# Kernel tuning notes

Hardware: AMD Instinct MI355X
Metric: run time of the kernel (lower is better)

## Reference

```python
import jax, jax.numpy as jnp
import numpy as np

KERNEL_SIZE = 11
SIGMA = 1.5
K1 = 0.01
K2 = 0.03
DATA_RANGE = 1.0


def _gaussian_kernel_2d(kernel_size=KERNEL_SIZE, sigma=SIGMA):
    x = jnp.arange(kernel_size, dtype=jnp.float32) - kernel_size // 2
    k1d = jnp.exp(-0.5 * (x / sigma) ** 2)
    k1d = k1d / k1d.sum()
    k2d = k1d[None, :] * k1d[:, None]
    # OIHW layout, single in/out channel
    return k2d[None, None, :, :]


def _gauss_filter(x, kernel):
    pad = KERNEL_SIZE // 2
    return jax.lax.conv_general_dilated(
        x, kernel,
        window_strides=(1, 1),
        padding=[(pad, pad), (pad, pad)],
        dimension_numbers=('NCHW', 'OIHW', 'NCHW'))


def setup_inputs() -> dict:
    key = jax.random.key(0)
    k1, k2 = jax.random.split(key)
    B, C, H, W = 128, 1, 320, 320
    pred = jax.random.uniform(k1, (B, C, H, W), dtype=jnp.float32)
    target = jax.random.uniform(k2, (B, C, H, W), dtype=jnp.float32)
    return {"pred": pred, "target": target}


def reference(pred, target):
    kernel = _gaussian_kernel_2d()
    mu_x = _gauss_filter(pred, kernel)
    mu_y = _gauss_filter(target, kernel)
    mu_x_sq = mu_x * mu_x
    mu_y_sq = mu_y * mu_y
    mu_xy = mu_x * mu_y
    sigma_x_sq = _gauss_filter(pred * pred, kernel) - mu_x_sq
    sigma_y_sq = _gauss_filter(target * target, kernel) - mu_y_sq
    sigma_xy = _gauss_filter(pred * target, kernel) - mu_xy
    dr = jnp.asarray(DATA_RANGE, dtype=pred.dtype)
    c1 = (K1 * dr) ** 2
    c2 = (K2 * dr) ** 2
    numerator = (2 * mu_xy + c1) * (2 * sigma_xy + c2)
    denominator = (mu_x_sq + mu_y_sq + c1) * (sigma_x_sq + sigma_y_sq + c2)
    ssim_map = numerator / denominator
    return 1.0 - ssim_map.mean()
```

## Files before the change

kernel.cpp:

```cpp
#include <hip/hip_runtime.h>


namespace {
constexpr int W = 320, H = 320, B = 128;
constexpr int TH = 8;
constexpr int NSTRIPE = H / TH;
constexpr int NWAVE = B * NSTRIPE;
constexpr int ITERS = TH / 2;
constexpr float C1 = 1.0e-4f;
constexpr float C2 = 9.0e-4f;
constexpr int NSLOT = 128;
constexpr int SSTR = 16;
}

typedef _Float16 h2 __attribute__((ext_vector_type(2)));
typedef float f4a __attribute__((ext_vector_type(4), aligned(4)));

__device__ __forceinline__ float fdot2f(h2 a, h2 b, float c) {
#if __has_builtin(__builtin_amdgcn_fdot2)
  return __builtin_amdgcn_fdot2(a, b, c, false);
#else
  return fmaf((float)a.x, (float)b.x, fmaf((float)a.y, (float)b.y, c));
#endif
}

__device__ __forceinline__ float rcpf(float x) {
  float r;
  asm("v_rcp_f32 %0, %1" : "=v"(r) : "v"(x));
  return r;
}

__device__ __forceinline__ h2 pack2(float a, float b) {
  return h2{(_Float16)a, (_Float16)b};
}

__device__ __forceinline__ h2 pkrtz(float a, float b) {
#if __has_builtin(__builtin_amdgcn_cvt_pkrtz)
  return __builtin_bit_cast(h2, __builtin_amdgcn_cvt_pkrtz(a, b));
#else
  return pack2(a, b);
#endif
}

__device__ __forceinline__ h2 dpp_up1(h2 v) {
  int r = __builtin_amdgcn_update_dpp(0, __builtin_bit_cast(int, v),
                                      0x138, 0xF, 0xF, true);
  return __builtin_bit_cast(h2, r);
}
__device__ __forceinline__ h2 dpp_dn1(h2 v) {
  int r = __builtin_amdgcn_update_dpp(0, __builtin_bit_cast(int, v),
                                      0x130, 0xF, 0xF, true);
  return __builtin_bit_cast(h2, r);
}

#define LOADROW_V(PTR, A)                                                     \
  do {                                                                        \
    const f4a q_ = *(const f4a*)(PTR);                                        \
    A[0] = q_.x; A[1] = q_.y; A[2] = q_.z; A[3] = q_.w;                       \
    A[4] = (PTR)[4];                                                          \
  } while (0)

#define LOADP_RAW(ROW, A0, B0, A1, B1)                                        \
  do {                                                                        \
    const int r0_ = (ROW);                                                    \
    if (r0_ >= 0 && r0_ < H) {                                                \
      LOADROW_V(P + r0_ * W, A0);                                             \
      LOADROW_V(T + r0_ * W, B0);                                             \
    } else {                                                                  \
      _Pragma("unroll") for (int c_ = 0; c_ < 5; ++c_) {                      \
        A0[c_] = 0.f; B0[c_] = 0.f;                                           \
      }                                                                       \
    }                                                                         \
    if (r0_ + 1 >= 0 && r0_ + 1 < H) {                                        \
      LOADROW_V(P + (r0_ + 1) * W, A1);                                       \
      LOADROW_V(T + (r0_ + 1) * W, B1);                                       \
    } else {                                                                  \
      _Pragma("unroll") for (int c_ = 0; c_ < 5; ++c_) {                      \
        A1[c_] = 0.f; B1[c_] = 0.f;                                           \
      }                                                                       \
    }                                                                         \
  } while (0)

#define PACKTO(J, A0, B0, A1, B1)                                             \
  do {                                                                        \
    _Pragma("unroll") for (int c_ = 0; c_ < 5; ++c_) {                        \
      const h2 hp_ = pkrtz(A0[c_], A1[c_]);                                   \
      const h2 ht_ = pkrtz(B0[c_], B1[c_]);                                   \
      rs[J][c_] = (hp_ + ht_) * H05;                                          \
      rd[J][c_] = (hp_ - ht_) * H05;                                          \
    }                                                                         \
  } while (0)

#define HALO(PKc, L, R)                                                       \
  do {                                                                        \
    _Pragma("unroll") for (int c_ = 0; c_ < 5; ++c_) {                        \
      L[c_] = dpp_up1(PKc[c_]);                                               \
      R[c_] = dpp_dn1(PKc[c_]);                                               \
    }                                                                         \
  } while (0)

#define XCOL(PKc, L, R, G)                                                    \
  (((G) < 0) ? L[(G) + 5] : (((G) <= 4) ? PKc[(G)] : R[(G) - 5]))

#define HBLUR9(PKc, L, R, O)                                                  \
  do {                                                                        \
    _Pragma("unroll") for (int c_ = 0; c_ < 5; ++c_) {                        \
      h2 s1_ = W9H[0] * XCOL(PKc, L, R, c_ - 4);                              \
      _Pragma("unroll") for (int k_ = 1; k_ <= 4; ++k_)                       \
        s1_ = W9H[k_] * XCOL(PKc, L, R, c_ - 4 + k_) + s1_;                   \
      h2 s2_ = W9H[8] * XCOL(PKc, L, R, c_ + 4);                              \
      _Pragma("unroll") for (int k_ = 7; k_ >= 5; --k_)                       \
        s2_ = W9H[k_] * XCOL(PKc, L, R, c_ - 4 + k_) + s2_;                   \
      O[c_] = s1_ + s2_;                                                      \
    }                                                                         \
  } while (0)

__global__ __launch_bounds__(64) void ssim_main(
    const float* __restrict__ pred, const float* __restrict__ targ,
    float* __restrict__ sink, int slotmask, int sstr) {
  const int lane = threadIdx.x & 63;
  const int stripe = blockIdx.x;
  const int img = stripe / NSTRIPE;
  const int y0  = (stripe % NSTRIPE) * TH;

  const float* __restrict__ P = pred + (size_t)img * (W * H) + 5 * lane;
  const float* __restrict__ T = targ + (size_t)img * (W * H) + 5 * lane;

  constexpr float W9[9] = {0.00761451f, 0.03607501f, 0.10958607f, 0.21344455f,
                           0.26655996f, 0.21344455f, 0.10958607f, 0.03607501f,
                           0.00761451f};
  const h2 wAv[5] = {pack2(W9[0], W9[1]), pack2(W9[2], W9[3]),
                     pack2(W9[4], W9[5]), pack2(W9[6], W9[7]),
                     pack2(W9[8], 0.f)};
  const h2 wBv[5] = {pack2(0.f, W9[0]),   pack2(W9[1], W9[2]),
                     pack2(W9[3], W9[4]), pack2(W9[5], W9[6]),
                     pack2(W9[7], W9[8])};
  h2 W9H[9];
#pragma unroll
  for (int k = 0; k < 9; ++k) W9H[k] = pack2(W9[k], W9[k]);
  const h2 H05 = pack2(0.5f, 0.5f);

  h2 rs[5][5], rd[5][5];
  float nfA[5], ntA[5], nfB[5], ntB[5];

  {
    float aA[5], bA[5], cA[5], dA[5];
    float aB[5], bB[5], cB[5], dB[5];
    LOADP_RAW(y0 - 4, aA, bA, cA, dA);
    LOADP_RAW(y0 - 2, aB, bB, cB, dB);
    PACKTO(1, aA, bA, cA, dA);
    LOADP_RAW(y0 + 0, aA, bA, cA, dA);
    PACKTO(2, aB, bB, cB, dB);
    LOADP_RAW(y0 + 2, aB, bB, cB, dB);
    PACKTO(3, aA, bA, cA, dA);
    LOADP_RAW(y0 + 4, nfA, ntA, nfB, ntB);
    PACKTO(4, aB, bB, cB, dB);
  }

  float acc = 0.f;

#pragma unroll 1
  for (int it = 0; it < ITERS; ++it) {
#pragma unroll
    for (int j = 0; j < 4; ++j)
#pragma unroll
      for (int c = 0; c < 5; ++c) {
        rs[j][c] = rs[j + 1][c];
        rd[j][c] = rd[j + 1][c];
      }
    PACKTO(4, nfA, ntA, nfB, ntB);
    if (it + 1 < ITERS) LOADP_RAW(y0 + 2 * it + 6, nfA, ntA, nfB, ntB);

    h2 PK[4][5];
#pragma unroll
    for (int c = 0; c < 5; ++c) {
      float sA = 0, dA = 0, ssA = 0, ddA = 0;
      float sB = 0, dB = 0, ssB = 0, ddB = 0;
#pragma unroll
      for (int j = 0; j < 5; ++j) {
        const h2 a = rs[j][c], b = rd[j][c];
        const h2 aa = a * a, bb = b * b;
        const h2 wa = wAv[j], wb = wBv[j];
        sA  = fdot2f(wa, a, sA);
        dA  = fdot2f(wa, b, dA);
        ssA = fdot2f(wa, aa, ssA);
        ddA = fdot2f(wa, bb, ddA);
        sB  = fdot2f(wb, a, sB);
        dB  = fdot2f(wb, b, dB);
        ssB = fdot2f(wb, aa, ssB);
        ddB = fdot2f(wb, bb, ddB);
      }
      PK[0][c] = pkrtz(sA, sB);
      PK[1][c] = pkrtz(dA, dB);
      PK[2][c] = pkrtz(ssA, ssB);
      PK[3][c] = pkrtz(ddA, ddB);
    }

    h2 OUT[4][5];
#pragma unroll
    for (int ch = 0; ch < 4; ++ch) {
      h2 L[5], R[5];
      HALO(PK[ch], L, R);
      HBLUR9(PK[ch], L, R, OUT[ch]);
    }

#pragma unroll
    for (int c = 0; c < 5; ++c) {
#pragma unroll
      for (int r = 0; r < 2; ++r) {
        const float u = r ? (float)OUT[0][c].y : (float)OUT[0][c].x;
        const float v = r ? (float)OUT[1][c].y : (float)OUT[1][c].x;
        const float w = r ? (float)OUT[2][c].y : (float)OUT[2][c].x;
        const float x = r ? (float)OUT[3][c].y : (float)OUT[3][c].x;
        const float uu = u * u, vv = v * v;
        const float A  = uu + vv;
        const float Bq = uu - vv;
        const float num1 = fmaf(2.f, Bq, C1);
        const float num2 = fmaf(2.f, (w - x) - Bq, C2);
        const float den1 = fmaf(2.f, A, C1);
        const float den2 = fmaf(2.f, (w + x) - A, C2);
        acc = fmaf(num1 * num2, rcpf(den1 * den2), acc);
      }
    }
  }

#pragma unroll
  for (int off = 32; off; off >>= 1) acc += __shfl_xor(acc, off, 64);
  if (lane == 0) atomicAdd(sink + (stripe & slotmask) * sstr, acc);
}

__global__ void ssim_final(const float* __restrict__ sink, int nslot, int sstr,
                           float* __restrict__ out) {
  const int tid = threadIdx.x;
  float v = 0.f;
  for (int s = tid; s < nslot; s += 64) v += sink[s * sstr];
#pragma unroll
  for (int off = 32; off; off >>= 1) v += __shfl_xor(v, off, 64);
  if (tid == 0) out[0] = 1.f - v / 13107200.f;
}

extern "C" void kernel_launch(void* const* d_in, const int* in_sizes, int n_in,
                              void* d_out, int out_size, void* d_ws, size_t ws_size,
                              hipStream_t stream) {
  (void)in_sizes; (void)n_in; (void)out_size;
  const float* pred = (const float*)d_in[0];
  const float* targ = (const float*)d_in[1];
  float* out = (float*)d_out;

  float* sink;
  int nslot, sstr;
  const size_t need = (size_t)NSLOT * SSTR * sizeof(float);
  if (ws_size >= need) {
    sink = (float*)d_ws;
    nslot = NSLOT;
    sstr = SSTR;
  } else {
    sink = out;
    nslot = 1;
    sstr = 0;
  }
  (void)hipMemsetAsync(sink, 0, nslot == 1 ? sizeof(float) : need, stream);
  ssim_main<<<dim3(NWAVE), dim3(64), 0, stream>>>(pred, targ, sink, nslot - 1, sstr);
  ssim_final<<<1, 64, 0, stream>>>(sink, nslot, sstr, out);
}
```

Before: 52.17 us.

## Move SSIM final math to packed fp16 and unroll row loop by two

The pointwise SSIM combination now runs on packed half2 operations instead of per-lane fp32. The 0.5 scaling moves from the pack step into the final formula, which removes multiplies from the pack stage. The row loop is restructured to compute two row-pairs per iteration with a 6-deep register window, so the register shift and prefetch happen half as often. The cost is fp16 range and precision risk in the squared and product terms, including possible overflow or accuracy loss for the sum-scaled values, plus higher register pressure.

```diff
diff --git a/kernel.cpp b/kernel.cpp
--- a/kernel.cpp
+++ b/kernel.cpp
@@ -6,7 +6,6 @@
 constexpr int TH = 8;
 constexpr int NSTRIPE = H / TH;
 constexpr int NWAVE = B * NSTRIPE;
-constexpr int ITERS = TH / 2;
 constexpr float C1 = 1.0e-4f;
 constexpr float C2 = 9.0e-4f;
 constexpr int NSLOT = 128;
@@ -86,8 +85,8 @@
     _Pragma("unroll") for (int c_ = 0; c_ < 5; ++c_) {                        \
       const h2 hp_ = pkrtz(A0[c_], A1[c_]);                                   \
       const h2 ht_ = pkrtz(B0[c_], B1[c_]);                                   \
-      rs[J][c_] = (hp_ + ht_) * H05;                                          \
-      rd[J][c_] = (hp_ - ht_) * H05;                                          \
+      rs[J][c_] = hp_ + ht_;                                                  \
+      rd[J][c_] = hp_ - ht_;                                                  \
     }                                                                         \
   } while (0)
 
@@ -112,6 +111,51 @@
       _Pragma("unroll") for (int k_ = 7; k_ >= 5; --k_)                       \
         s2_ = W9H[k_] * XCOL(PKc, L, R, c_ - 4 + k_) + s2_;                   \
       O[c_] = s1_ + s2_;                                                      \
+    }                                                                         \
+  } while (0)
+
+#define COMPUTE(I)                                                            \
+  do {                                                                        \
+    h2 PK[4][5];                                                              \
+    _Pragma("unroll") for (int c = 0; c < 5; ++c) {                           \
+      float sA = 0, dA = 0, ssA = 0, ddA = 0;                                 \
+      float sB = 0, dB = 0, ssB = 0, ddB = 0;                                 \
+      _Pragma("unroll") for (int j = 0; j < 5; ++j) {                         \
+        const h2 a = rs[(I) + j][c], b = rd[(I) + j][c];                      \
+        const h2 aa = a * a, bb = b * b;                                      \
+        const h2 wa = wAv[j], wb = wBv[j];                                    \
+        sA  = fdot2f(wa, a, sA);                                              \
+        dA  = fdot2f(wa, b, dA);                                              \
+        ssA = fdot2f(wa, aa, ssA);                                            \
+        ddA = fdot2f(wa, bb, ddA);                                            \
+        sB  = fdot2f(wb, a, sB);                                              \
+        dB  = fdot2f(wb, b, dB);                                              \
+        ssB = fdot2f(wb, aa, ssB);                                            \
+        ddB = fdot2f(wb, bb, ddB);                                            \
+      }                                                                       \
+      PK[0][c] = pkrtz(sA, sB);                                               \
+      PK[1][c] = pkrtz(dA, dB);                                               \
+      PK[2][c] = pkrtz(ssA, ssB);                                             \
+      PK[3][c] = pkrtz(ddA, ddB);                                             \
+    }                                                                         \
+    h2 OUT[4][5];                                                             \
+    _Pragma("unroll") for (int ch = 0; ch < 4; ++ch) {                        \
+      h2 L[5], R[5];                                                          \
+      HALO(PK[ch], L, R);                                                     \
+      HBLUR9(PK[ch], L, R, OUT[ch]);                                          \
+    }                                                                         \
+    _Pragma("unroll") for (int c = 0; c < 5; ++c) {                           \
+      const h2 U = OUT[0][c], V = OUT[1][c];                                  \
+      const h2 w_ = OUT[2][c], x_ = OUT[3][c];                                \
+      const h2 uu = U * U, vv = V * V;                                        \
+      const h2 Ap = uu + vv, Bq = uu - vv;                                    \
+      const h2 n1 = Bq * HALFp + C1p;                          \
+      const h2 n2 = ((w_ - x_) - Bq) * HALFp + C2p;            \
+      const h2 d1 = Ap * HALFp + C1p;                          \
+      const h2 d2 = ((w_ + x_) - Ap) * HALFp + C2p;            \
+      const h2 NU = n1 * n2, DE = d1 * d2;                                    \
+      acc = fmaf((float)NU.x, rcpf((float)DE.x), acc);                        \
+      acc = fmaf((float)NU.y, rcpf((float)DE.y), acc);                        \
     }                                                                         \
   } while (0)
 
@@ -138,89 +182,49 @@
   h2 W9H[9];
 #pragma unroll
   for (int k = 0; k < 9; ++k) W9H[k] = pack2(W9[k], W9[k]);
-  const h2 H05 = pack2(0.5f, 0.5f);
-
-  h2 rs[5][5], rd[5][5];
-  float nfA[5], ntA[5], nfB[5], ntB[5];
+  const h2 HALFp = pack2(0.5f, 0.5f);
+  const h2 C1p = pack2(C1, C1);
+  const h2 C2p = pack2(C2, C2);
+
+  h2 rs[6][5], rd[6][5];
 
   {
     float aA[5], bA[5], cA[5], dA[5];
     float aB[5], bB[5], cB[5], dB[5];
     LOADP_RAW(y0 - 4, aA, bA, cA, dA);
     LOADP_RAW(y0 - 2, aB, bB, cB, dB);
-    PACKTO(1, aA, bA, cA, dA);
+    PACKTO(0, aA, bA, cA, dA);
     LOADP_RAW(y0 + 0, aA, bA, cA, dA);
-    PACKTO(2, aB, bB, cB, dB);
+    PACKTO(1, aB, bB, cB, dB);
     LOADP_RAW(y0 + 2, aB, bB, cB, dB);
-    PACKTO(3, aA, bA, cA, dA);
-    LOADP_RAW(y0 + 4, nfA, ntA, nfB, ntB);
-    PACKTO(4, aB, bB, cB, dB);
+    PACKTO(2, aA, bA, cA, dA);
+    LOADP_RAW(y0 + 4, aA, bA, cA, dA);
+    PACKTO(3, aB, bB, cB, dB);
+    LOADP_RAW(y0 + 6, aB, bB, cB, dB);
+    PACKTO(4, aA, bA, cA, dA);
+    PACKTO(5, aB, bB, cB, dB);
   }
 
   float acc = 0.f;
+  float nfA[5], ntA[5], nfB[5], ntB[5];
+  float mfA[5], mtA[5], mfB[5], mtB[5];
 
 #pragma unroll 1
-  for (int it = 0; it < ITERS; ++it) {
-#pragma unroll
-    for (int j = 0; j < 4; ++j)
-#pragma unroll
-      for (int c = 0; c < 5; ++c) {
-        rs[j][c] = rs[j + 1][c];
-        rd[j][c] = rd[j + 1][c];
-      }
-    PACKTO(4, nfA, ntA, nfB, ntB);
-    if (it + 1 < ITERS) LOADP_RAW(y0 + 2 * it + 6, nfA, ntA, nfB, ntB);
-
-    h2 PK[4][5];
-#pragma unroll
-    for (int c = 0; c < 5; ++c) {
-      float sA = 0, dA = 0, ssA = 0, ddA = 0;
-      float sB = 0, dB = 0, ssB = 0, ddB = 0;
-#pragma unroll
-      for (int j = 0; j < 5; ++j) {
-        const h2 a = rs[j][c], b = rd[j][c];
-        const h2 aa = a * a, bb = b * b;
-        const h2 wa = wAv[j], wb = wBv[j];
-        sA  = fdot2f(wa, a, sA);
-        dA  = fdot2f(wa, b, dA);
-        ssA = fdot2f(wa, aa, ssA);
-        ddA = fdot2f(wa, bb, ddA);
-        sB  = fdot2f(wb, a, sB);
-        dB  = fdot2f(wb, b, dB);
-        ssB = fdot2f(wb, aa, ssB);
-        ddB = fdot2f(wb, bb, ddB);
-      }
-      PK[0][c] = pkrtz(sA, sB);
-      PK[1][c] = pkrtz(dA, dB);
-      PK[2][c] = pkrtz(ssA, ssB);
-      PK[3][c] = pkrtz(ddA, ddB);
-    }
-
-    h2 OUT[4][5];
-#pragma unroll
-    for (int ch = 0; ch < 4; ++ch) {
-      h2 L[5], R[5];
-      HALO(PK[ch], L, R);
-      HBLUR9(PK[ch], L, R, OUT[ch]);
-    }
-
-#pragma unroll
-    for (int c = 0; c < 5; ++c) {
-#pragma unroll
-      for (int r = 0; r < 2; ++r) {
-        const float u = r ? (float)OUT[0][c].y : (float)OUT[0][c].x;
-        const float v = r ? (float)OUT[1][c].y : (float)OUT[1][c].x;
-        const float w = r ? (float)OUT[2][c].y : (float)OUT[2][c].x;
-        const float x = r ? (float)OUT[3][c].y : (float)OUT[3][c].x;
-        const float uu = u * u, vv = v * v;
-        const float A  = uu + vv;
-        const float Bq = uu - vv;
-        const float num1 = fmaf(2.f, Bq, C1);
-        const float num2 = fmaf(2.f, (w - x) - Bq, C2);
-        const float den1 = fmaf(2.f, A, C1);
-        const float den2 = fmaf(2.f, (w + x) - A, C2);
-        acc = fmaf(num1 * num2, rcpf(den1 * den2), acc);
-      }
+  for (int b = 0; b < 2; ++b) {
+    if (b == 0) LOADP_RAW(y0 + 8, nfA, ntA, nfB, ntB);
+    COMPUTE(0);
+    if (b == 0) LOADP_RAW(y0 + 10, mfA, mtA, mfB, mtB);
+    COMPUTE(1);
+    if (b == 0) {
+#pragma unroll
+      for (int j = 0; j < 4; ++j)
+#pragma unroll
+        for (int c = 0; c < 5; ++c) {
+          rs[j][c] = rs[j + 2][c];
+          rd[j][c] = rd[j + 2][c];
+        }
+      PACKTO(4, nfA, ntA, nfB, ntB);
+      PACKTO(5, mfA, mtA, mfB, mtB);
     }
   }
 
```

Result: faster. 50.08 us (-4.0%).
